# Performance work log

Hardware: AMD Instinct MI355X
Metric: run time of the kernel (lower is better)

Reference implementation:

```python
import jax, jax.numpy as jnp
import numpy as np

B, S, D, F, H, R, BLK = 1, 2048, 1024, 2816, 16, 16, 64
DH = D // H  # 64

# bitsandbytes NF4 codebook
NF4_CODE = jnp.array([-1.0, -0.6961928009986877, -0.5250730514526367, -0.39491748809814453,
                      -0.28444138169288635, -0.18477343022823334, -0.09105003625154495, 0.0,
                      0.07958029955625534, 0.16093020141124725, 0.24611230194568634, 0.33791524171829224,
                      0.44070982933044434, 0.5626170039176941, 0.7229568362236023, 1.0], dtype=jnp.float32)


def dequant_nf4(codes, absmax, shape):
    # blockwise NF4 dequant: codebook lookup * per-64-element absmax scale
    w = NF4_CODE[codes.reshape(-1)]
    return (w.reshape(-1, BLK) * absmax[:, None]).reshape(shape)


def rmsnorm(x, w, eps=1e-10):
    return x * jax.lax.rsqrt(jnp.mean(x * x, axis=-1, keepdims=True) + eps) * w


def rotate_half(x):
    x1, x2 = jnp.split(x, 2, axis=-1)
    return jnp.concatenate((-x2, x1), axis=-1)


def apply_rope(x, cos, sin, pos):
    # x: [B,H,S,DH], pos: [B,S] -> gather rope tables per position
    c = cos[pos][:, None]  # [B,1,S,DH]
    s = sin[pos][:, None]
    return x * c + rotate_half(x) * s


def proj(x, codes, absmax, la, lb, shape):
    # fused NF4 dequant-matmul + additive LoRA branch: x @ W.T + (x @ A) @ B
    w = dequant_nf4(codes, absmax, shape)
    return x @ w.T + (x @ la) @ lb


def _forward(x, nw1, nw2, cos, sin,
             qa, qla, qlb, ka, kla, klb, va, vla, vlb, oa, ola, olb,
             ga, gla, glb, ua, ula, ulb, da, dla, dlb,
             pos, qc, kc, vc, oc, gc, uc, dc):
    h1 = rmsnorm(x, nw1)
    q = proj(h1, qc, qa, qla, qlb, (D, D))
    k = proj(h1, kc, ka, kla, klb, (D, D))
    v = proj(h1, vc, va, vla, vlb, (D, D))

    def heads(t):
        return t.reshape(B, S, H, DH).transpose(0, 2, 1, 3)

    q = apply_rope(heads(q), cos, sin, pos)
    k = apply_rope(heads(k), cos, sin, pos)
    v = heads(v)

    scores = jnp.einsum('bhqd,bhkd->bhqk', q, k) / np.float32(np.sqrt(DH))
    causal = jnp.tril(jnp.ones((S, S), dtype=bool))
    mask = jnp.where(causal, 0.0, -1e9).astype(scores.dtype)  # additive attention_mask
    attn = jax.nn.softmax(scores + mask, axis=-1)
    o = jnp.einsum('bhqk,bhkd->bhqd', attn, v).transpose(0, 2, 1, 3).reshape(B, S, D)
    o = proj(o, oc, oa, ola, olb, (D, D))

    x1 = x + o  # first residual
    h2 = rmsnorm(x1, nw2)
    gate = proj(h2, gc, ga, gla, glb, (F, D))
    up = proj(h2, uc, ua, ula, ulb, (F, D))
    had = up * jax.nn.silu(gate)  # SwiGLU hadamard
    down = proj(had, dc, da, dla, dlb, (D, F))
    return x1 + down


def setup_inputs():
    ks = iter(jax.random.split(jax.random.key(0), 48))

    def rn(shape, scale=1.0):
        return jax.random.normal(next(ks), shape, jnp.float32) * scale

    def cd(shape):
        return jax.random.randint(next(ks), shape, 0, 16, dtype=jnp.int32)

    def am(n):
        return jax.random.uniform(next(ks), (n,), jnp.float32) * 0.04 + 0.01

    inp = {'x': rn((B, S, D)),
           'norm_weight_1': 1.0 + rn((D,), 0.02),
           'norm_weight_2': 1.0 + rn((D,), 0.02)}
    inv = 1.0 / (10000.0 ** (jnp.arange(0, DH, 2, dtype=jnp.float32) / DH))
    ang = jnp.arange(S, dtype=jnp.float32)[:, None] * inv[None, :]
    emb = jnp.concatenate((ang, ang), axis=-1)  # [S, DH]
    inp['cos'], inp['sin'] = jnp.cos(emb), jnp.sin(emb)
    inp['position_ids'] = jnp.broadcast_to(jnp.arange(S, dtype=jnp.int32), (B, S))
    shapes = {'q': (D, D), 'k': (D, D), 'v': (D, D), 'o': (D, D),
              'gate': (F, D), 'up': (F, D), 'down': (D, F)}
    for p, (o, i) in shapes.items():
        inp['w_%s_codes' % p] = cd((o, i))
        inp['w_%s_absmax' % p] = am(o * i // BLK)
        inp['w_%s_lora_a' % p] = rn((i, R), 1.0 / np.sqrt(i))
        inp['w_%s_lora_b' % p] = rn((R, o), 0.01)
    return inp


def reference(x, norm_weight_1, norm_weight_2, cos, sin, position_ids,
              w_q_codes, w_q_absmax, w_q_lora_a, w_q_lora_b,
              w_k_codes, w_k_absmax, w_k_lora_a, w_k_lora_b,
              w_v_codes, w_v_absmax, w_v_lora_a, w_v_lora_b,
              w_o_codes, w_o_absmax, w_o_lora_a, w_o_lora_b,
              w_gate_codes, w_gate_absmax, w_gate_lora_a, w_gate_lora_b,
              w_up_codes, w_up_absmax, w_up_lora_a, w_up_lora_b,
              w_down_codes, w_down_absmax, w_down_lora_a, w_down_lora_b):
    return _forward(x, norm_weight_1, norm_weight_2, cos, sin,
                    w_q_absmax, w_q_lora_a, w_q_lora_b,
                    w_k_absmax, w_k_lora_a, w_k_lora_b,
                    w_v_absmax, w_v_lora_a, w_v_lora_b,
                    w_o_absmax, w_o_lora_a, w_o_lora_b,
                    w_gate_absmax, w_gate_lora_a, w_gate_lora_b,
                    w_up_absmax, w_up_lora_a, w_up_lora_b,
                    w_down_absmax, w_down_lora_a, w_down_lora_b,
                    position_ids, w_q_codes, w_k_codes, w_v_codes,
                    w_o_codes, w_gate_codes, w_up_codes, w_down_codes)
```

## Files before the change

### kernel.cpp

```cpp
#include <hip/hip_runtime.h>
#include <stdint.h>


#define Sq   2048
#define Dm   1024
#define Fm   2816
#define Hh   16
#define LH   1120
#define KQ   1088
#define LGU  1056
#define LO   1120
#define KO   1088
#define LD   2912
#define KD   2880
#define NQKV 3072
#define NGU  5632

typedef short bf16x8 __attribute__((ext_vector_type(8)));
typedef float f32x4  __attribute__((ext_vector_type(4)));

__constant__ float NF4_LUT[16] = {
    -1.0f, -0.6961928009986877f, -0.5250730514526367f, -0.39491748809814453f,
    -0.28444138169288635f, -0.18477343022823334f, -0.09105003625154495f, 0.0f,
    0.07958029955625534f, 0.16093020141124725f, 0.24611230194568634f,
    0.33791524171829224f, 0.44070982933044434f, 0.5626170039176941f,
    0.7229568362236023f, 1.0f};

__device__ inline unsigned short f2bf(float f) {
    union { float f; uint32_t u; } v; v.f = f;
    uint32_t u = v.u;
    return (unsigned short)((u + 0x7FFFu + ((u >> 16) & 1u)) >> 16);
}
__device__ inline float bf2f(unsigned short h) {
    union { uint32_t u; float f; } v; v.u = ((uint32_t)h) << 16;
    return v.f;
}
__device__ inline unsigned short truncbf(float f) {
    union { float f; uint32_t u; } v; v.f = f;
    return (unsigned short)(v.u >> 16);
}

#define GLD16(gp, lp)                                                         \
    __builtin_amdgcn_global_load_lds(                                         \
        (__attribute__((address_space(1))) void*)(uintptr_t)(gp),             \
        (__attribute__((address_space(3))) void*)(uint32_t)(uintptr_t)(lp),   \
        16, 0, 0)

__global__ __launch_bounds__(256) void rmsnorm_ext(
    const float* __restrict__ X, const float* __restrict__ W,
    unsigned short* Hout, int ldh)
{
    int s = blockIdx.x, tid = threadIdx.x;
    const float4 v = *(const float4*)(X + (size_t)s * Dm + tid * 4);
    float ss = v.x * v.x + v.y * v.y + v.z * v.z + v.w * v.w;
#pragma unroll
    for (int m = 1; m < 64; m <<= 1) ss += __shfl_xor(ss, m);
    __shared__ float red[4];
    int lane = tid & 63, wave = tid >> 6;
    if (lane == 0) red[wave] = ss;
    __syncthreads();
    float scale = rsqrtf((red[0] + red[1] + red[2] + red[3]) * (1.0f / Dm) + 1e-10f);
    const float4 w = *(const float4*)(W + tid * 4);
    alignas(8) unsigned short o[4];
    o[0] = f2bf(v.x * scale * w.x);
    o[1] = f2bf(v.y * scale * w.y);
    o[2] = f2bf(v.z * scale * w.z);
    o[3] = f2bf(v.w * scale * w.w);
    *(ushort4*)(Hout + (size_t)s * ldh + tid * 4) = *(ushort4*)o;
    if (tid < 64) Hout[(size_t)s * ldh + Dm + tid] = 0;
}

__global__ __launch_bounds__(256) void lora_prep(
    const float* __restrict__ qla, const float* __restrict__ kla,
    const float* __restrict__ vla, const float* __restrict__ ola,
    const float* __restrict__ gla, const float* __restrict__ ula,
    const float* __restrict__ dla, unsigned short* __restrict__ lapk)
{
    int tid = threadIdx.x;
    int chunk = blockIdx.x * 4 + (tid >> 6);
    int lane = tid & 63;
    int lr = lane & 15, quad = lane >> 4;
    const float* la;
    int lc;
    if (chunk < 192) {
        int m = chunk >> 5; lc = chunk & 31;
        la = (m == 0) ? qla : (m == 1) ? kla : (m == 2) ? vla
           : (m == 3) ? ola : (m == 4) ? gla : ula;
    } else {
        la = dla; lc = chunk - 192;
    }
    alignas(16) unsigned short out[8];
#pragma unroll
    for (int e = 0; e < 8; ++e)
        out[e] = f2bf(la[(size_t)(lc * 32 + quad * 8 + e) * 16 + lr]);
    *(uint4*)(lapk + (size_t)chunk * 512 + lane * 8) = *(uint4*)out;
}

template<int NM>
__global__ __launch_bounds__(256) void lora_mfma(
    unsigned short* Aext, int lda, int K,
    const unsigned short* __restrict__ lapk, int c0, int c1, int c2,
    int toff, int zoff, int zn)
{
    int tid = threadIdx.x;
    int lane = tid & 63, wave = tid >> 6;
    int lr = lane & 15, quad = lane >> 4;
    int r0 = blockIdx.x * 16;
    int nc4 = K >> 7;
    int gc0 = wave * nc4;
    const unsigned short* Ab = Aext + (size_t)(r0 + lr) * lda + quad * 8;
    int cb[3] = {c0, c1, c2};
    f32x4 zero = {0.f, 0.f, 0.f, 0.f};
    f32x4 acc[NM];
#pragma unroll
    for (int m = 0; m < NM; ++m) acc[m] = zero;
    for (int cc = 0; cc < nc4; ++cc) {
        int gc = gc0 + cc;
        bf16x8 af = *(const bf16x8*)(Ab + gc * 32);
#pragma unroll
        for (int m = 0; m < NM; ++m) {
            bf16x8 bf = *(const bf16x8*)(lapk + (size_t)(cb[m] + gc) * 512 + lane * 8);
            acc[m] = __builtin_amdgcn_mfma_f32_16x16x32_bf16(af, bf, acc[m], 0, 0, 0);
        }
    }
    __shared__ float red[3][NM * 64 * 4];
    if (wave > 0) {
#pragma unroll
        for (int m = 0; m < NM; ++m)
#pragma unroll
            for (int r = 0; r < 4; ++r)
                red[wave - 1][(m * 64 + lane) * 4 + r] = acc[m][r];
    }
    __syncthreads();
    if (wave == 0) {
#pragma unroll
        for (int m = 0; m < NM; ++m)
#pragma unroll
            for (int r = 0; r < 4; ++r)
                acc[m][r] += red[0][(m * 64 + lane) * 4 + r]
                           + red[1][(m * 64 + lane) * 4 + r]
                           + red[2][(m * 64 + lane) * 4 + r];
#pragma unroll
        for (int r = 0; r < 4; ++r) {
            int row = r0 + quad * 4 + r;
#pragma unroll
            for (int m = 0; m < NM; ++m)
                Aext[(size_t)row * lda + toff + m * 16 + lr] = f2bf(acc[m][r]);
        }
        if (zn > 0) {
            int row = r0 + lr, j0 = quad * 4;
            for (int j = j0; j < zn; j += 64) {
                alignas(8) unsigned short z4[4] = {0, 0, 0, 0};
                *(ushort4*)(Aext + (size_t)row * lda + zoff + j) = *(ushort4*)z4;
            }
        }
    }
}

__device__ inline void dq_row8(const float* lut, const int* cod, const float* am,
                               const float* lb, int nr, int c8, int K, int Nlb,
                               int toff, unsigned short* out)
{
    if (c8 < K) {
        size_t base = (size_t)nr * K + c8;
        const int4* cp = (const int4*)(cod + base);
        int4 ca = cp[0], cb = cp[1];
        float a = am[base >> 6];
        out[0] = f2bf(lut[ca.x] * a); out[1] = f2bf(lut[ca.y] * a);
        out[2] = f2bf(lut[ca.z] * a); out[3] = f2bf(lut[ca.w] * a);
        out[4] = f2bf(lut[cb.x] * a); out[5] = f2bf(lut[cb.y] * a);
        out[6] = f2bf(lut[cb.z] * a); out[7] = f2bf(lut[cb.w] * a);
    } else {
        int r = c8 - toff;
#pragma unroll
        for (int i = 0; i < 8; ++i) out[i] = 0;
        if (r >= 0 && r < 16) {
#pragma unroll
            for (int i = 0; i < 8; ++i) out[i] = f2bf(lb[(size_t)(r + i) * Nlb + nr]);
        }
    }
}

__global__ __launch_bounds__(256) void dequant_qkv(
    const int* __restrict__ qc, const int* __restrict__ kc, const int* __restrict__ vc,
    const float* __restrict__ qa, const float* __restrict__ ka, const float* __restrict__ va,
    const float* __restrict__ qlb, const float* __restrict__ klb, const float* __restrict__ vlb,
    unsigned short* __restrict__ Wout)
{
    __shared__ float lut[16];
    if (threadIdx.x < 16) lut[threadIdx.x] = NF4_LUT[threadIdx.x];
    __syncthreads();
    int idx = blockIdx.x * 256 + threadIdx.x;
    int n = idx / 140;
    int c8 = (idx - n * 140) * 8;
    int seg = n >> 10, nr = n & 1023;
    const int* cod   = (seg == 0) ? qc : (seg == 1) ? kc : vc;
    const float* am  = (seg == 0) ? qa : (seg == 1) ? ka : va;
    const float* lb  = (seg == 0) ? qlb : (seg == 1) ? klb : vlb;
    int toff = 1024 + (seg << 4);
    alignas(16) unsigned short out[8];
    dq_row8(lut, cod, am, lb, nr, c8, 1024, 1024, toff, out);
    *(uint4*)(Wout + (size_t)n * LH + c8) = *(uint4*)out;
}

__global__ __launch_bounds__(256) void dequant_gu(
    const int* __restrict__ gc, const int* __restrict__ uc,
    const float* __restrict__ ga, const float* __restrict__ ua,
    const float* __restrict__ glb, const float* __restrict__ ulb,
    unsigned short* __restrict__ Wout)
{
    __shared__ float lut[16];
    if (threadIdx.x < 16) lut[threadIdx.x] = NF4_LUT[threadIdx.x];
    __syncthreads();
    int idx = blockIdx.x * 256 + threadIdx.x;
    int n = idx / 132;
    int c8 = (idx - n * 132) * 8;
    int m = n >> 1, mat = n & 1;
    const int* cod  = mat ? uc : gc;
    const float* am = mat ? ua : ga;
    const float* lb = mat ? ulb : glb;
    int toff = 1024 + (mat << 4);
    alignas(16) unsigned short out[8];
    dq_row8(lut, cod, am, lb, m, c8, 1024, Fm, toff, out);
    *(uint4*)(Wout + (size_t)n * LGU + c8) = *(uint4*)out;
}

__global__ __launch_bounds__(256) void dequant_ext(
    const int* __restrict__ codes, const float* __restrict__ absmax,
    const float* __restrict__ lb, unsigned short* __restrict__ Wout,
    int Nproj, int K, int ldw, int toff)
{
    __shared__ float lut[16];
    if (threadIdx.x < 16) lut[threadIdx.x] = NF4_LUT[threadIdx.x];
    __syncthreads();
    int idx = blockIdx.x * 256 + threadIdx.x;
    int cpr = ldw >> 3;
    int n = idx / cpr;
    if (n >= Nproj) return;
    int c8 = (idx - n * cpr) * 8;
    alignas(16) unsigned short out[8];
    dq_row8(lut, codes, absmax, lb, n, c8, K, Nproj, toff, out);
    *(uint4*)(Wout + (size_t)n * ldw + c8) = *(uint4*)out;
}

__global__ __launch_bounds__(256) void gemm128(
    const unsigned short* __restrict__ A, int lda,
    const unsigned short* __restrict__ B, int ldb, int K,
    unsigned short* __restrict__ Cb, int ldc)
{
    __shared__ __align__(16) unsigned short At[2][128 * 32];
    __shared__ __align__(16) unsigned short Bt[2][128 * 32];
    int tid = threadIdx.x;
    int lane = tid & 63, wave = tid >> 6;
    int lr = lane & 15, quad = lane >> 4;
    int wm = (wave >> 1) * 64, wn = (wave & 1) * 64;
    int row0 = blockIdx.y * 128, col0 = blockIdx.x * 128;
    f32x4 acc[4][4];
    f32x4 zero = {0.f, 0.f, 0.f, 0.f};
#pragma unroll
    for (int i = 0; i < 4; ++i)
#pragma unroll
        for (int j = 0; j < 4; ++j) acc[i][j] = zero;
    int sw = ((tid & 3) ^ ((tid >> 3) & 3)) * 8;
    const unsigned short* Ag  = A + (size_t)(row0 + (tid >> 2)) * lda + sw;
    const unsigned short* Ag2 = Ag + (size_t)64 * lda;
    const unsigned short* Bg  = B + (size_t)(col0 + (tid >> 2)) * ldb + sw;
    const unsigned short* Bg2 = Bg + (size_t)64 * ldb;
    int l0 = tid * 8, l1 = (tid + 256) * 8;
    GLD16(Ag, At[0] + l0); GLD16(Ag2, At[0] + l1);
    GLD16(Bg, Bt[0] + l0); GLD16(Bg2, Bt[0] + l1);
    int sq = (quad ^ ((lr >> 1) & 3)) * 8;
    int nIter = K >> 5;
    for (int it = 0; it < nIter; ++it) {
        int cur = it & 1;
        __syncthreads();
        if (it + 1 < nIter) {
            int k = (it + 1) << 5, nx = cur ^ 1;
            GLD16(Ag + k, At[nx] + l0); GLD16(Ag2 + k, At[nx] + l1);
            GLD16(Bg + k, Bt[nx] + l0); GLD16(Bg2 + k, Bt[nx] + l1);
        }
        bf16x8 af[4], bfr[4];
#pragma unroll
        for (int i = 0; i < 4; ++i)
            af[i] = *(const bf16x8*)(At[cur] + (wm + i * 16 + lr) * 32 + sq);
#pragma unroll
        for (int j = 0; j < 4; ++j)
            bfr[j] = *(const bf16x8*)(Bt[cur] + (wn + j * 16 + lr) * 32 + sq);
#pragma unroll
        for (int i = 0; i < 4; ++i)
#pragma unroll
            for (int j = 0; j < 4; ++j)
                acc[i][j] = __builtin_amdgcn_mfma_f32_16x16x32_bf16(af[i], bfr[j], acc[i][j], 0, 0, 0);
    }
#pragma unroll
    for (int i = 0; i < 4; ++i) {
        int rowb = row0 + wm + i * 16 + quad * 4;
#pragma unroll
        for (int j = 0; j < 4; ++j) {
            int col = col0 + wn + j * 16 + lr;
#pragma unroll
            for (int r = 0; r < 4; ++r)
                Cb[(size_t)(rowb + r) * ldc + col] = f2bf(acc[i][j][r]);
        }
    }
}

__global__ __launch_bounds__(256) void gemm_gu(
    const unsigned short* __restrict__ A, int lda,
    const unsigned short* __restrict__ B, int ldb, int K,
    unsigned short* __restrict__ Hb)
{
    __shared__ __align__(16) unsigned short At[2][128 * 32];
    __shared__ __align__(16) unsigned short Bt[2][128 * 32];
    int tid = threadIdx.x;
    int lane = tid & 63, wave = tid >> 6;
    int lr = lane & 15, quad = lane >> 4;
    int wm = (wave >> 1) * 64, wn = (wave & 1) * 64;
    int row0 = blockIdx.y * 128, col0 = blockIdx.x * 128;
    f32x4 acc[4][4];
    f32x4 zero = {0.f, 0.f, 0.f, 0.f};
#pragma unroll
    for (int i = 0; i < 4; ++i)
#pragma unroll
        for (int j = 0; j < 4; ++j) acc[i][j] = zero;
    int sw = ((tid & 3) ^ ((tid >> 3) & 3)) * 8;
    const unsigned short* Ag  = A + (size_t)(row0 + (tid >> 2)) * lda + sw;
    const unsigned short* Ag2 = Ag + (size_t)64 * lda;
    const unsigned short* Bg  = B + (size_t)(col0 + (tid >> 2)) * ldb + sw;
    const unsigned short* Bg2 = Bg + (size_t)64 * ldb;
    int l0 = tid * 8, l1 = (tid + 256) * 8;
    GLD16(Ag, At[0] + l0); GLD16(Ag2, At[0] + l1);
    GLD16(Bg, Bt[0] + l0); GLD16(Bg2, Bt[0] + l1);
    int sq = (quad ^ ((lr >> 1) & 3)) * 8;
    int nIter = K >> 5;
    for (int it = 0; it < nIter; ++it) {
        int cur = it & 1;
        __syncthreads();
        if (it + 1 < nIter) {
            int k = (it + 1) << 5, nx = cur ^ 1;
            GLD16(Ag + k, At[nx] + l0); GLD16(Ag2 + k, At[nx] + l1);
            GLD16(Bg + k, Bt[nx] + l0); GLD16(Bg2 + k, Bt[nx] + l1);
        }
        bf16x8 af[4], bfr[4];
#pragma unroll
        for (int i = 0; i < 4; ++i)
            af[i] = *(const bf16x8*)(At[cur] + (wm + i * 16 + lr) * 32 + sq);
#pragma unroll
        for (int j = 0; j < 4; ++j)
            bfr[j] = *(const bf16x8*)(Bt[cur] + (wn + j * 16 + lr) * 32 + sq);
#pragma unroll
        for (int i = 0; i < 4; ++i)
#pragma unroll
            for (int j = 0; j < 4; ++j)
                acc[i][j] = __builtin_amdgcn_mfma_f32_16x16x32_bf16(af[i], bfr[j], acc[i][j], 0, 0, 0);
    }
#pragma unroll
    for (int i = 0; i < 4; ++i) {
        int rowb = row0 + wm + i * 16 + quad * 4;
#pragma unroll
        for (int j = 0; j < 4; ++j) {
            int col = col0 + wn + j * 16 + lr;
#pragma unroll
            for (int r = 0; r < 4; ++r) {
                float own = acc[i][j][r];
                float oth = __shfl_xor(own, 1);
                if (!(lr & 1)) {
                    float sig = 1.0f / (1.0f + __expf(-own));
                    Hb[(size_t)(rowb + r) * LD + (col >> 1)] = f2bf(oth * own * sig);
                }
            }
        }
    }
}

template<int TAG>
__global__ __launch_bounds__(256) void gemm_s(
    const unsigned short* __restrict__ A, int lda,
    const unsigned short* __restrict__ B, int ldb, int K,
    float* __restrict__ Cf, int ldc, const float* __restrict__ Radd)
{
    __shared__ __align__(16) unsigned short At[2][64 * 64];
    __shared__ __align__(16) unsigned short Bt[2][64 * 64];
    int tid = threadIdx.x;
    int lane = tid & 63, wave = tid >> 6;
    int lr = lane & 15, quad = lane >> 4;
    int row0 = blockIdx.y * 64, col0 = blockIdx.x * 64;
    f32x4 acc[4];
    f32x4 zero = {0.f, 0.f, 0.f, 0.f};
#pragma unroll
    for (int j = 0; j < 4; ++j) acc[j] = zero;
    int rs = tid >> 3;
    int g8 = ((tid & 7) ^ (rs & 7)) * 8;
    const unsigned short* Ag  = A + (size_t)(row0 + rs) * lda + g8;
    const unsigned short* Ag2 = Ag + (size_t)32 * lda;
    const unsigned short* Bg  = B + (size_t)(col0 + rs) * ldb + g8;
    const unsigned short* Bg2 = Bg + (size_t)32 * ldb;
    int l0 = tid * 8, l1 = (tid + 256) * 8;
    GLD16(Ag, At[0] + l0); GLD16(Ag2, At[0] + l1);
    GLD16(Bg, Bt[0] + l0); GLD16(Bg2, Bt[0] + l1);
    int c0 = (quad ^ (lr & 7)) * 8;
    int c1 = ((4 + quad) ^ (lr & 7)) * 8;
    int nIter = K >> 6;
    for (int it = 0; it < nIter; ++it) {
        int cur = it & 1;
        __syncthreads();
        if (it + 1 < nIter) {
            int k = (it + 1) << 6, nx = cur ^ 1;
            GLD16(Ag + k, At[nx] + l0); GLD16(Ag2 + k, At[nx] + l1);
            GLD16(Bg + k, Bt[nx] + l0); GLD16(Bg2 + k, Bt[nx] + l1);
        }
        const unsigned short* arow = At[cur] + (wave * 16 + lr) * 64;
        bf16x8 a0 = *(const bf16x8*)(arow + c0);
        bf16x8 a1 = *(const bf16x8*)(arow + c1);
        bf16x8 b0[4], b1[4];
#pragma unroll
        for (int j = 0; j < 4; ++j) {
            const unsigned short* brow = Bt[cur] + (j * 16 + lr) * 64;
            b0[j] = *(const bf16x8*)(brow + c0);
            b1[j] = *(const bf16x8*)(brow + c1);
        }
#pragma unroll
        for (int j = 0; j < 4; ++j) {
            acc[j] = __builtin_amdgcn_mfma_f32_16x16x32_bf16(a0, b0[j], acc[j], 0, 0, 0);
            acc[j] = __builtin_amdgcn_mfma_f32_16x16x32_bf16(a1, b1[j], acc[j], 0, 0, 0);
        }
    }
    int rowb = row0 + wave * 16 + quad * 4;
#pragma unroll
    for (int j = 0; j < 4; ++j) {
        int col = col0 + j * 16 + lr;
#pragma unroll
        for (int r = 0; r < 4; ++r) {
            size_t o = (size_t)(rowb + r) * ldc + col;
            Cf[o] = acc[j][r] + Radd[o];
        }
    }
}

__global__ __launch_bounds__(256) void rope_pack(
    const unsigned short* __restrict__ qkv,
    const float* __restrict__ cosT, const float* __restrict__ sinT,
    const int* __restrict__ pos,
    unsigned short* __restrict__ qb, unsigned short* __restrict__ kpk,
    unsigned short* __restrict__ vpk)
{
    int b = blockIdx.x, tid = threadIdx.x;
    if (b < 8192) {
        int idx = b * 256 + tid;
        int s = idx >> 10, col = idx & 1023, d = col & 63;
        int p = pos[s];
        float c = cosT[p * 64 + d], sn = sinT[p * 64 + d];
        int partner = (d < 32) ? (col + 32) : (col - 32);
        float sgn = (d < 32) ? -1.f : 1.f;
        const unsigned short* row = qkv + (size_t)s * NQKV;
        float q = bf2f(row[col]), q2 = bf2f(row[partner]);
        qb[idx] = f2bf((q * c + sgn * q2 * sn) * 0.125f);
    } else if (b < 9216) {
        int g = (b - 8192) * 256 + tid;
        int lr = g & 15, quad = (g >> 4) & 3, cch = (g >> 6) & 1;
        int t = (g >> 7) & 127, h = g >> 14;
        int s = t * 16 + lr;
        int p = pos[s];
        int d0 = cch * 32 + quad * 8;
        const unsigned short* krow = qkv + (size_t)s * NQKV + Dm + h * 64;
        uint4 kv8 = *(const uint4*)(krow + d0);
        uint4 kp8 = *(const uint4*)(krow + ((d0 + 32) & 63));
        float sgn = (d0 < 32) ? -1.f : 1.f;
        const float* cp = cosT + p * 64 + d0;
        const float* sp = sinT + p * 64 + d0;
        const unsigned short* ke = (const unsigned short*)&kv8;
        const unsigned short* pe = (const unsigned short*)&kp8;
        alignas(16) unsigned short out[8];
#pragma unroll
        for (int e = 0; e < 8; ++e)
            out[e] = f2bf(bf2f(ke[e]) * cp[e] + sgn * bf2f(pe[e]) * sp[e]);
        *(uint4*)(kpk + (size_t)g * 8) = *(uint4*)out;
    } else {
        int g = (b - 9216) * 256 + tid;
        int lrr = g & 15, quad = (g >> 4) & 3, kk = (g >> 6) & 3;
        int j = (g >> 8) & 3, kt = (g >> 10) & 15, h = g >> 14;
        int d = j * 16 + lrr;
        int sbase = kt * 128 + kk * 32 + quad * 8;
        alignas(16) unsigned short out[8];
#pragma unroll
        for (int e = 0; e < 8; ++e)
            out[e] = qkv[(size_t)(sbase + e) * NQKV + 2048 + h * 64 + d];
        *(uint4*)(vpk + (size_t)g * 8) = *(uint4*)out;
    }
}

__global__ __launch_bounds__(256) void attn(
    const unsigned short* __restrict__ qb, const unsigned short* __restrict__ kpk,
    const unsigned short* __restrict__ vpk, unsigned short* __restrict__ ob)
{
    __shared__ __align__(16) unsigned short Ps[4][16 * 136];
    int tid = threadIdx.x;
    int lane = tid & 63, wave = tid >> 6;
    int lr = lane & 15, quad = lane >> 4;
    int idx = blockIdx.x;
    int t_ = idx >> 4;
    int qt = (idx < 256) ? (31 - t_) : (t_ - 16);
    int h = idx & 15;
    int r0 = qt * 64 + wave * 16;
    const unsigned short* qp = qb + (size_t)(r0 + lr) * Dm + h * 64 + quad * 8;
    bf16x8 qf0 = *(const bf16x8*)qp;
    bf16x8 qf1 = *(const bf16x8*)(qp + 32);
    const unsigned short* kpb = kpk + (size_t)h * 128 * 1024 + lane * 8;
    const unsigned short* vpb = vpk + (size_t)h * 16 * 16 * 512 + lane * 8;
    f32x4 zero = {0.f, 0.f, 0.f, 0.f};
    f32x4 oacc[4];
#pragma unroll
    for (int j = 0; j < 4; ++j) oacc[j] = zero;
    float lrow[4] = {0.f, 0.f, 0.f, 0.f};
    int ntile = (qt * 64 + 191) >> 7;

    for (int kt = 0; kt < ntile; ++kt) {
        int k0 = kt << 7;
        f32x4 sf[8];
#pragma unroll
        for (int jj = 0; jj < 8; ++jj) {
            const unsigned short* kp = kpb + (size_t)(kt * 8 + jj) * 1024;
            bf16x8 kf0 = *(const bf16x8*)kp;
            bf16x8 kf1 = *(const bf16x8*)(kp + 512);
            f32x4 z = zero;
            z = __builtin_amdgcn_mfma_f32_16x16x32_bf16(qf0, kf0, z, 0, 0, 0);
            z = __builtin_amdgcn_mfma_f32_16x16x32_bf16(qf1, kf1, z, 0, 0, 0);
            sf[jj] = z;
        }
        bf16x8 vf[4][4];
#pragma unroll
        for (int j = 0; j < 4; ++j)
#pragma unroll
            for (int kk = 0; kk < 4; ++kk)
                vf[j][kk] = *(const bf16x8*)(vpb + (size_t)((kt * 4 + j) * 4 + kk) * 512);
        if (kt == ntile - 1) {
#pragma unroll
            for (int jj = 0; jj < 8; ++jj)
#pragma unroll
                for (int r = 0; r < 4; ++r)
                    if (k0 + jj * 16 + lr > r0 + quad * 4 + r)
                        sf[jj][r] = -1e30f;
        }
#pragma unroll
        for (int jj = 0; jj < 8; ++jj)
#pragma unroll
            for (int r = 0; r < 4; ++r) {
                float p = __expf(sf[jj][r]);
                sf[jj][r] = p;
                lrow[r] += p;
            }
#pragma unroll
        for (int jj = 0; jj < 8; ++jj)
#pragma unroll
            for (int r = 0; r < 4; ++r)
                Ps[wave][(quad * 4 + r) * 136 + jj * 16 + lr] = truncbf(sf[jj][r]);
        bf16x8 pf[4];
#pragma unroll
        for (int kk = 0; kk < 4; ++kk)
            pf[kk] = *(const bf16x8*)(&Ps[wave][lr * 136 + kk * 32 + quad * 8]);
#pragma unroll
        for (int j = 0; j < 4; ++j)
#pragma unroll
            for (int kk = 0; kk < 4; ++kk)
                oacc[j] = __builtin_amdgcn_mfma_f32_16x16x32_bf16(pf[kk], vf[j][kk], oacc[j], 0, 0, 0);
    }
#pragma unroll
    for (int r = 0; r < 4; ++r)
#pragma unroll
        for (int m = 1; m < 16; m <<= 1) lrow[r] += __shfl_xor(lrow[r], m);
#pragma unroll
    for (int r = 0; r < 4; ++r) {
        float inv = 1.0f / lrow[r];
        int row = r0 + quad * 4 + r;
#pragma unroll
        for (int j = 0; j < 4; ++j)
            ob[(size_t)row * LO + h * 64 + j * 16 + lr] = f2bf(oacc[j][r] * inv);
    }
}

extern "C" void kernel_launch(void* const* d_in, const int* in_sizes, int n_in,
                              void* d_out, int out_size, void* d_ws, size_t ws_size,
                              hipStream_t stream)
{
    const float* x    = (const float*)d_in[0];
    const float* nw1  = (const float*)d_in[1];
    const float* nw2  = (const float*)d_in[2];
    const float* cosT = (const float*)d_in[3];
    const float* sinT = (const float*)d_in[4];
    const int*   pos  = (const int*)d_in[5];
    const int   *qc = (const int*)d_in[6],  *kc = (const int*)d_in[10],
                *vc = (const int*)d_in[14], *oc = (const int*)d_in[18],
                *gc = (const int*)d_in[22], *uc = (const int*)d_in[26],
                *dc = (const int*)d_in[30];
    const float *qa = (const float*)d_in[7],  *ka = (const float*)d_in[11],
                *va = (const float*)d_in[15], *oa = (const float*)d_in[19],
                *ga = (const float*)d_in[23], *ua = (const float*)d_in[27],
                *da = (const float*)d_in[31];
    const float *qla = (const float*)d_in[8],  *kla = (const float*)d_in[12],
                *vla = (const float*)d_in[16], *ola = (const float*)d_in[20],
                *gla = (const float*)d_in[24], *ula = (const float*)d_in[28],
                *dla = (const float*)d_in[32];
    const float *qlb = (const float*)d_in[9],  *klb = (const float*)d_in[13],
                *vlb = (const float*)d_in[17], *olb = (const float*)d_in[21],
                *glb = (const float*)d_in[25], *ulb = (const float*)d_in[29],
                *dlb = (const float*)d_in[33];

    char* ws = (char*)d_ws;
    unsigned short* h    = (unsigned short*)(ws + 0);
    unsigned short* W    = (unsigned short*)(ws + 4587520);
    unsigned short* qkv  = (unsigned short*)(ws + 16482304);
    unsigned short* qbf  = (unsigned short*)(ws + 29065216);
    unsigned short* kpk  = (unsigned short*)(ws + 33259520);
    unsigned short* vpk  = (unsigned short*)(ws + 37453824);
    unsigned short* obf  = (unsigned short*)(ws + 41648128);
    float*          x1   = (float*)(ws + 29065216);
    unsigned short* hb   = (unsigned short*)(ws + 46235648);
    unsigned short* lapk = (unsigned short*)(ws + 58163200);
    float* outp = (float*)d_out;

    lora_prep<<<70, 256, 0, stream>>>(qla, kla, vla, ola, gla, ula, dla, lapk);
    rmsnorm_ext<<<Sq, 256, 0, stream>>>(x, nw1, h, LH);
    lora_mfma<3><<<128, 256, 0, stream>>>(h, LH, Dm, lapk, 0, 32, 64, 1024, 0, 0);
    dequant_qkv<<<1680, 256, 0, stream>>>(qc, kc, vc, qa, ka, va, qlb, klb, vlb, W);
    gemm128<<<dim3(NQKV / 128, Sq / 128), 256, 0, stream>>>(h, LH, W, LH, KQ, qkv, NQKV);
    rope_pack<<<10240, 256, 0, stream>>>(qkv, cosT, sinT, pos, qbf, kpk, vpk);
    attn<<<512, 256, 0, stream>>>(qbf, kpk, vpk, obf);
    lora_mfma<1><<<128, 256, 0, stream>>>(obf, LO, Dm, lapk, 96, 0, 0, 1024, 1040, 48);
    dequant_ext<<<560, 256, 0, stream>>>(oc, oa, olb, W, Dm, Dm, LO, 1024);
    gemm_s<0><<<dim3(Dm / 64, Sq / 64), 256, 0, stream>>>(obf, LO, W, LO, KO, x1, Dm, x);
    rmsnorm_ext<<<Sq, 256, 0, stream>>>(x1, nw2, h, LH);
    lora_mfma<2><<<128, 256, 0, stream>>>(h, LH, Dm, lapk, 128, 160, 0, 1024, 0, 0);
    dequant_gu<<<2904, 256, 0, stream>>>(gc, uc, ga, ua, glb, ulb, W);
    gemm_gu<<<dim3(NGU / 128, Sq / 128), 256, 0, stream>>>(h, LH, W, LGU, LGU, hb);
    lora_mfma<1><<<128, 256, 0, stream>>>(hb, LD, Fm, lapk, 192, 0, 0, 2816, 2848, 32);
    dequant_ext<<<1456, 256, 0, stream>>>(dc, da, dlb, W, Dm, Fm, LD, 2816);
    gemm_s<1><<<dim3(Dm / 64, Sq / 64), 256, 0, stream>>>(hb, LD, W, LD, KD, outp, Dm, x1);
}
```

Baseline: 348.7 us.

## Tighten activation strides and stage K/V packing through shared memory

```diff
diff --git a/kernel.cpp b/kernel.cpp
--- a/kernel.cpp
+++ b/kernel.cpp
@@ -6,12 +6,12 @@
 #define Dm   1024
 #define Fm   2816
 #define Hh   16
-#define LH   1120
+#define LHA  1088
+#define LWQ  1120
 #define KQ   1088
 #define LGU  1056
-#define LO   1120
-#define KO   1088
-#define LD   2912
+#define LHB  2880
+#define LWD  2912
 #define KD   2880
 #define NQKV 3072
 #define NGU  5632
@@ -200,7 +200,7 @@
     int toff = 1024 + (seg << 4);
     alignas(16) unsigned short out[8];
     dq_row8(lut, cod, am, lb, nr, c8, 1024, 1024, toff, out);
-    *(uint4*)(Wout + (size_t)n * LH + c8) = *(uint4*)out;
+    *(uint4*)(Wout + (size_t)n * LWQ + c8) = *(uint4*)out;
 }
 
 __global__ __launch_bounds__(256) void dequant_gu(
@@ -366,7 +366,7 @@
                 float oth = __shfl_xor(own, 1);
                 if (!(lr & 1)) {
                     float sig = 1.0f / (1.0f + __expf(-own));
-                    Hb[(size_t)(rowb + r) * LD + (col >> 1)] = f2bf(oth * own * sig);
+                    Hb[(size_t)(rowb + r) * LHB + (col >> 1)] = f2bf(oth * own * sig);
                 }
             }
         }
@@ -444,6 +444,7 @@
     unsigned short* __restrict__ qb, unsigned short* __restrict__ kpk,
     unsigned short* __restrict__ vpk)
 {
+    __shared__ __align__(16) unsigned short t[128][72];
     int b = blockIdx.x, tid = threadIdx.x;
     if (b < 8192) {
         int idx = b * 256 + tid;
@@ -455,37 +456,65 @@
         const unsigned short* row = qkv + (size_t)s * NQKV;
         float q = bf2f(row[col]), q2 = bf2f(row[partner]);
         qb[idx] = f2bf((q * c + sgn * q2 * sn) * 0.125f);
-    } else if (b < 9216) {
-        int g = (b - 8192) * 256 + tid;
-        int lr = g & 15, quad = (g >> 4) & 3, cch = (g >> 6) & 1;
-        int t = (g >> 7) & 127, h = g >> 14;
-        int s = t * 16 + lr;
-        int p = pos[s];
-        int d0 = cch * 32 + quad * 8;
-        const unsigned short* krow = qkv + (size_t)s * NQKV + Dm + h * 64;
-        uint4 kv8 = *(const uint4*)(krow + d0);
-        uint4 kp8 = *(const uint4*)(krow + ((d0 + 32) & 63));
-        float sgn = (d0 < 32) ? -1.f : 1.f;
-        const float* cp = cosT + p * 64 + d0;
-        const float* sp = sinT + p * 64 + d0;
-        const unsigned short* ke = (const unsigned short*)&kv8;
-        const unsigned short* pe = (const unsigned short*)&kp8;
-        alignas(16) unsigned short out[8];
-#pragma unroll
-        for (int e = 0; e < 8; ++e)
-            out[e] = f2bf(bf2f(ke[e]) * cp[e] + sgn * bf2f(pe[e]) * sp[e]);
-        *(uint4*)(kpk + (size_t)g * 8) = *(uint4*)out;
+    } else if (b < 8448) {
+        int bb = b - 8192;
+        int h = bb >> 4, sb = bb & 15;
+        int s0 = sb * 128;
+#pragma unroll
+        for (int p = 0; p < 4; ++p) {
+            int flat = p * 256 + tid;
+            int row = flat >> 3, c8 = (flat & 7) * 8;
+            *(uint4*)&t[row][c8] =
+                *(const uint4*)(qkv + (size_t)(s0 + row) * NQKV + Dm + h * 64 + c8);
+        }
+        __syncthreads();
+        int lane = tid & 63, fw = tid >> 6;
+        int lr = lane & 15, quad = lane >> 4;
+#pragma unroll
+        for (int ff = 0; ff < 4; ++ff) {
+            int frag = fw * 4 + ff;
+            int t16 = frag >> 1, c = frag & 1;
+            int srow = t16 * 16 + lr;
+            int p2 = pos[s0 + srow];
+            int d0 = c * 32 + quad * 8;
+            float sgn = (d0 < 32) ? -1.f : 1.f;
+            const float* cp = cosT + p2 * 64 + d0;
+            const float* sp = sinT + p2 * 64 + d0;
+            alignas(16) unsigned short out[8];
+#pragma unroll
+            for (int e = 0; e < 8; ++e) {
+                float kv = bf2f(t[srow][d0 + e]);
+                float kq = bf2f(t[srow][(d0 + e) ^ 32]);
+                out[e] = f2bf(kv * cp[e] + sgn * kq * sp[e]);
+            }
+            size_t fbase = ((size_t)(h * 128 + sb * 8 + t16) * 2 + c) * 512;
+            *(uint4*)(kpk + fbase + lane * 8) = *(uint4*)out;
+        }
     } else {
-        int g = (b - 9216) * 256 + tid;
-        int lrr = g & 15, quad = (g >> 4) & 3, kk = (g >> 6) & 3;
-        int j = (g >> 8) & 3, kt = (g >> 10) & 15, h = g >> 14;
-        int d = j * 16 + lrr;
-        int sbase = kt * 128 + kk * 32 + quad * 8;
-        alignas(16) unsigned short out[8];
-#pragma unroll
-        for (int e = 0; e < 8; ++e)
-            out[e] = qkv[(size_t)(sbase + e) * NQKV + 2048 + h * 64 + d];
-        *(uint4*)(vpk + (size_t)g * 8) = *(uint4*)out;
+        int bb = b - 8448;
+        int h = bb >> 4, kt = bb & 15;
+        int s0 = kt * 128;
+#pragma unroll
+        for (int p = 0; p < 4; ++p) {
+            int flat = p * 256 + tid;
+            int row = flat >> 3, c8 = (flat & 7) * 8;
+            *(uint4*)&t[row][c8] =
+                *(const uint4*)(qkv + (size_t)(s0 + row) * NQKV + 2048 + h * 64 + c8);
+        }
+        __syncthreads();
+        int lane = tid & 63, fw = tid >> 6;
+        int lr = lane & 15, quad = lane >> 4;
+#pragma unroll
+        for (int ff = 0; ff < 4; ++ff) {
+            int frag = fw * 4 + ff;
+            int j = frag >> 2, kk = frag & 3;
+            alignas(16) unsigned short out[8];
+#pragma unroll
+            for (int e = 0; e < 8; ++e)
+                out[e] = t[kk * 32 + quad * 8 + e][j * 16 + lr];
+            size_t fbase = (size_t)(((h * 16 + kt) * 4 + j) * 4 + kk) * 512;
+            *(uint4*)(vpk + fbase + lane * 8) = *(uint4*)out;
+        }
     }
 }
 
@@ -574,7 +603,7 @@
         int row = r0 + quad * 4 + r;
 #pragma unroll
         for (int j = 0; j < 4; ++j)
-            ob[(size_t)row * LO + h * 64 + j * 16 + lr] = f2bf(oacc[j][r] * inv);
+            ob[(size_t)row * LHA + h * 64 + j * 16 + lr] = f2bf(oacc[j][r] * inv);
     }
 }
 
@@ -607,32 +636,32 @@
 
     char* ws = (char*)d_ws;
     unsigned short* h    = (unsigned short*)(ws + 0);
-    unsigned short* W    = (unsigned short*)(ws + 4587520);
-    unsigned short* qkv  = (unsigned short*)(ws + 16482304);
-    unsigned short* qbf  = (unsigned short*)(ws + 29065216);
-    unsigned short* kpk  = (unsigned short*)(ws + 33259520);
-    unsigned short* vpk  = (unsigned short*)(ws + 37453824);
-    unsigned short* obf  = (unsigned short*)(ws + 41648128);
-    float*          x1   = (float*)(ws + 29065216);
-    unsigned short* hb   = (unsigned short*)(ws + 46235648);
-    unsigned short* lapk = (unsigned short*)(ws + 58163200);
+    unsigned short* W    = (unsigned short*)(ws + 4456448);
+    unsigned short* qkv  = (unsigned short*)(ws + 16351232);
+    unsigned short* qbf  = (unsigned short*)(ws + 28934144);
+    unsigned short* kpk  = (unsigned short*)(ws + 33128448);
+    unsigned short* vpk  = (unsigned short*)(ws + 37322752);
+    unsigned short* obf  = (unsigned short*)(ws + 41517056);
+    float*          x1   = (float*)(ws + 28934144);
+    unsigned short* hb   = (unsigned short*)(ws + 45973504);
+    unsigned short* lapk = (unsigned short*)(ws + 57769984);
     float* outp = (float*)d_out;
 
     lora_prep<<<70, 256, 0, stream>>>(qla, kla, vla, ola, gla, ula, dla, lapk);
-    rmsnorm_ext<<<Sq, 256, 0, stream>>>(x, nw1, h, LH);
-    lora_mfma<3><<<128, 256, 0, stream>>>(h, LH, Dm, lapk, 0, 32, 64, 1024, 0, 0);
+    rmsnorm_ext<<<Sq, 256, 0, stream>>>(x, nw1, h, LHA);
+    lora_mfma<3><<<128, 256, 0, stream>>>(h, LHA, Dm, lapk, 0, 32, 64, 1024, 0, 0);
     dequant_qkv<<<1680, 256, 0, stream>>>(qc, kc, vc, qa, ka, va, qlb, klb, vlb, W);
-    gemm128<<<dim3(NQKV / 128, Sq / 128), 256, 0, stream>>>(h, LH, W, LH, KQ, qkv, NQKV);
-    rope_pack<<<10240, 256, 0, stream>>>(qkv, cosT, sinT, pos, qbf, kpk, vpk);
+    gemm128<<<dim3(NQKV / 128, Sq / 128), 256, 0, stream>>>(h, LHA, W, LWQ, KQ, qkv, NQKV);
+    rope_pack<<<8704, 256, 0, stream>>>(qkv, cosT, sinT, pos, qbf, kpk, vpk);
     attn<<<512, 256, 0, stream>>>(qbf, kpk, vpk, obf);
-    lora_mfma<1><<<128, 256, 0, stream>>>(obf, LO, Dm, lapk, 96, 0, 0, 1024, 1040, 48);
-    dequant_ext<<<560, 256, 0, stream>>>(oc, oa, olb, W, Dm, Dm, LO, 1024);
-    gemm_s<0><<<dim3(Dm / 64, Sq / 64), 256, 0, stream>>>(obf, LO, W, LO, KO, x1, Dm, x);
-    rmsnorm_ext<<<Sq, 256, 0, stream>>>(x1, nw2, h, LH);
-    lora_mfma<2><<<128, 256, 0, stream>>>(h, LH, Dm, lapk, 128, 160, 0, 1024, 0, 0);
+    lora_mfma<1><<<128, 256, 0, stream>>>(obf, LHA, Dm, lapk, 96, 0, 0, 1024, 1040, 48);
+    dequant_ext<<<560, 256, 0, stream>>>(oc, oa, olb, W, Dm, Dm, LWQ, 1024);
+    gemm_s<0><<<dim3(Dm / 64, Sq / 64), 256, 0, stream>>>(obf, LHA, W, LWQ, KQ, x1, Dm, x);
+    rmsnorm_ext<<<Sq, 256, 0, stream>>>(x1, nw2, h, LHA);
+    lora_mfma<2><<<128, 256, 0, stream>>>(h, LHA, Dm, lapk, 128, 160, 0, 1024, 0, 0);
     dequant_gu<<<2904, 256, 0, stream>>>(gc, uc, ga, ua, glb, ulb, W);
-    gemm_gu<<<dim3(NGU / 128, Sq / 128), 256, 0, stream>>>(h, LH, W, LGU, LGU, hb);
-    lora_mfma<1><<<128, 256, 0, stream>>>(hb, LD, Fm, lapk, 192, 0, 0, 2816, 2848, 32);
-    dequant_ext<<<1456, 256, 0, stream>>>(dc, da, dlb, W, Dm, Fm, LD, 2816);
-    gemm_s<1><<<dim3(Dm / 64, Sq / 64), 256, 0, stream>>>(hb, LD, W, LD, KD, outp, Dm, x1);
-}
+    gemm_gu<<<dim3(NGU / 128, Sq / 128), 256, 0, stream>>>(h, LHA, W, LGU, LGU, hb);
+    lora_mfma<1><<<128, 256, 0, stream>>>(hb, LHB, Fm, lapk, 192, 0, 0, 2816, 2832, 48);
+    dequant_ext<<<1456, 256, 0, stream>>>(dc, da, dlb, W, Dm, Fm, LWD, 2816);
+    gemm_s<1><<<dim3(Dm / 64, Sq / 64), 256, 0, stream>>>(hb, LHB, W, LWD, KD, outp, Dm, x1);
+}
```

New measurement: 358.9 us. 1.03x slower.
